# Optimization experiments

Measured on AMD Instinct MI355X. Metric: run time of the kernel, lower is better.

Reference implementation:

```python
import jax, jax.numpy as jnp
import numpy as np

H = 2880      # hidden_size
I = 2880      # intermediate_size
E = 8         # num_experts
K = 4         # experts_per_token
N = 1024      # num tokens
EPS = 1e-5
ALPHA = 1.702
BETA = 1.0


def setup_inputs() -> dict:
    key = jax.random.key(0)
    ks = jax.random.split(key, 8)
    s = 0.02
    return {
        "x": jax.random.normal(ks[0], (N, H), jnp.float32),
        "norm_w": jnp.ones((H,), jnp.float32),
        "gate_w": jax.random.normal(ks[1], (E, H), jnp.float32) * s,
        "gate_b": jax.random.normal(ks[2], (E,), jnp.float32) * s,
        "w_gate_up": jax.random.normal(ks[3], (E, 2 * I, H), jnp.float32) * s,
        "b_gate_up": jax.random.normal(ks[4], (E, 2 * I), jnp.float32) * s,
        "w_down": jax.random.normal(ks[5], (E, H, I), jnp.float32) * s,
        "b_down": jax.random.normal(ks[6], (E, H), jnp.float32) * s,
    }


def reference(x, norm_w, gate_w, gate_b, w_gate_up, b_gate_up, w_down, b_down):
    # RMSNorm
    t = x * jax.lax.rsqrt(jnp.mean(x * x, axis=-1, keepdims=True) + EPS) * norm_w
    # Router gate (Linear with bias)
    logits = t @ gate_w.T + gate_b                      # [N, E]
    # Renormalize routing: top-k of logits, softmax over selected logits
    top_vals, top_idx = jax.lax.top_k(logits, K)        # [N, K]
    route_w = jax.nn.softmax(top_vals, axis=-1)         # [N, K]
    # Dense combine matrix [N, E] (zero for unselected experts)
    n_ar = jnp.arange(N)[:, None]
    R = jnp.zeros((N, E), t.dtype).at[n_ar, top_idx].add(route_w)
    # Fused gate_up projection per expert: [E, N, 2I]
    h = jnp.einsum('nh,eih->eni', t, w_gate_up) + b_gate_up[:, None, :]
    x_glu, x_lin = h[..., :I], h[..., I:]
    # SwiGLU with per-expert alpha/beta (all 1.702 / 1.0)
    act = x_glu * jax.nn.sigmoid(ALPHA * x_glu) * (x_lin + BETA)   # [E, N, I]
    # Down projection per expert: [E, N, H]
    outs = jnp.einsum('eni,ehi->enh', act, w_down) + b_down[:, None, :]
    # Weighted combine over selected experts + residual
    y = jnp.einsum('ne,enh->nh', R, outs)
    return x + y
```

## Files before the change

### kernel.cpp

```cpp
#include <hip/hip_runtime.h>
#include <hip/hip_bf16.h>

#define NTOK 1024
#define HDIM 2880
#define IDIM 2880
#define NEXP 8
#define BK 64
#define NT 45

typedef __attribute__((ext_vector_type(4))) float fx4;
typedef __attribute__((ext_vector_type(8))) short sx8;
typedef __attribute__((ext_vector_type(8))) unsigned short usx8;

typedef const __attribute__((address_space(1))) void* gas_p;
typedef __attribute__((address_space(3))) void* las_p;

__device__ __forceinline__ unsigned short f2bf(float f) {
  __hip_bfloat16 b = __float2bfloat16(f);
  return __builtin_bit_cast(unsigned short, b);
}
__device__ __forceinline__ usx8 cvt8(fx4 a, fx4 b) {
  usx8 u = {f2bf(a.x), f2bf(a.y), f2bf(a.z), f2bf(a.w),
            f2bf(b.x), f2bf(b.y), f2bf(b.z), f2bf(b.w)};
  return u;
}
__device__ __forceinline__ float bf2f(unsigned short u) {
  unsigned v = ((unsigned)u) << 16;
  return __builtin_bit_cast(float, v);
}

#define MFMA16(a, b, c) __builtin_amdgcn_mfma_f32_16x16x32_bf16(a, b, c, 0, 0, 0)

__global__ __launch_bounds__(256) void rms_router_k(
    const float* __restrict__ x, const float* __restrict__ norm_w,
    const float* __restrict__ gate_w, const float* __restrict__ gate_b,
    unsigned short* __restrict__ t_bf, int* __restrict__ cnt,
    int* __restrict__ tok, int* __restrict__ tokE, int* __restrict__ tokS,
    float* __restrict__ tokW) {
  const int n = blockIdx.x;
  const int tid = threadIdx.x;
  const int wid = tid >> 6, lane = tid & 63;
  const float* xr = x + (size_t)n * HDIM;

  float ss = 0.f;
  for (int h = tid; h < HDIM; h += 256) { float v = xr[h]; ss += v * v; }
  #pragma unroll
  for (int o = 32; o > 0; o >>= 1) ss += __shfl_down(ss, o);
  __shared__ float sred[4];
  if (lane == 0) sred[wid] = ss;
  __syncthreads();
  const float rstd =
      rsqrtf((sred[0] + sred[1] + sred[2] + sred[3]) * (1.0f / HDIM) + 1e-5f);

  float p[NEXP];
  #pragma unroll
  for (int e = 0; e < NEXP; e++) p[e] = 0.f;
  for (int h = tid; h < HDIM; h += 256) {
    float xv = xr[h] * norm_w[h];
    t_bf[(size_t)n * HDIM + h] = f2bf(xv * rstd);
    #pragma unroll
    for (int e = 0; e < NEXP; e++) p[e] += xv * gate_w[e * HDIM + h];
  }
  __shared__ float pls[4][NEXP];
  #pragma unroll
  for (int e = 0; e < NEXP; e++) {
    float v = p[e];
    #pragma unroll
    for (int o = 32; o > 0; o >>= 1) v += __shfl_down(v, o);
    if (lane == 0) pls[wid][e] = v;
  }
  __syncthreads();
  if (tid == 0) {
    float lg[NEXP];
    #pragma unroll
    for (int e = 0; e < NEXP; e++)
      lg[e] = (pls[0][e] + pls[1][e] + pls[2][e] + pls[3][e]) * rstd + gate_b[e];
    unsigned used = 0;
    float val[4];
    int idx[4];
    for (int k = 0; k < 4; k++) {
      float best = -1e30f;
      int bi = 0;
      for (int e = 0; e < NEXP; e++)
        if (!((used >> e) & 1u) && lg[e] > best) { best = lg[e]; bi = e; }
      used |= 1u << bi;
      val[k] = best;
      idx[k] = bi;
    }
    float sum = 0.f, w[4];
    for (int k = 0; k < 4; k++) { w[k] = expf(val[k] - val[0]); sum += w[k]; }
    for (int k = 0; k < 4; k++) {
      int e = idx[k];
      int slot = atomicAdd(&cnt[e], 1);
      tok[e * NTOK + slot] = n;
      tokE[n * 4 + k] = e;
      tokS[n * 4 + k] = slot;
      tokW[n * 4 + k] = w[k] / sum;
    }
  }
}

__global__ __launch_bounds__(256) void pack_k(
    const unsigned short* __restrict__ t_bf, const int* __restrict__ cnt,
    const int* __restrict__ tok, unsigned short* __restrict__ a_pack) {
  const int e = blockIdx.x >> 8;
  const int r0 = (blockIdx.x & 255) * 4;
  const int ce = cnt[e];
  const int lim = (ce + 127) & ~127;
  if (r0 >= lim) return;
  const int row = r0 + (threadIdx.x >> 6);
  const int lane = threadIdx.x & 63;
  unsigned short* dst = a_pack + ((size_t)e * NTOK + row) * HDIM;
  if (row < ce) {
    const unsigned short* src = t_bf + (size_t)tok[e * NTOK + row] * HDIM;
    for (int c = lane; c < HDIM / 8; c += 64)
      *(usx8*)(dst + c * 8) = *(const usx8*)(src + c * 8);
  } else {
    const usx8 z = {0, 0, 0, 0, 0, 0, 0, 0};
    for (int c = lane; c < HDIM / 8; c += 64) *(usx8*)(dst + c * 8) = z;
  }
}

__global__ __launch_bounds__(256, 3) void gemm1_k(
    const unsigned short* __restrict__ a_pack,
    const float* __restrict__ w_gate_up, const float* __restrict__ b_gate_up,
    const int* __restrict__ cnt, unsigned short* __restrict__ act_bf) {
  const int h = blockIdx.x;
  const int u = (h >> 6) * 8 + (h & 7);
  const int z = (h >> 3) & 7;
  const int e = u / 45;
  const int c0 = (u % 45) * 64;
  const int m0 = z * 128;
  const int ce = cnt[e];
  if (m0 >= ce) return;

  const int tid = threadIdx.x, lane = tid & 63, wid = tid >> 6;
  const int fr = lane & 15, fq = lane >> 4;
  const int wm = wid >> 1, wn = wid & 1;
  const int sw = ((lane & 7) ^ ((lane >> 3) & 7)) * 8;

  __shared__ __align__(16) unsigned short Ash[128 * 64];
  __shared__ __align__(16) unsigned short Bsh[128 * 64];

  const fx4 FZ = {0.f, 0.f, 0.f, 0.f};
  fx4 accG[4][2], accL[4][2];
  #pragma unroll
  for (int m = 0; m < 4; m++)
    #pragma unroll
    for (int n = 0; n < 2; n++) { accG[m][n] = FZ; accL[m][n] = FZ; }

  const unsigned short* gA[4];
  #pragma unroll
  for (int j = 0; j < 4; ++j) {
    int row = m0 + wid * 32 + j * 8 + (lane >> 3);
    gA[j] = a_pack + ((size_t)e * NTOK + row) * HDIM + sw;
  }
  const float* fB[4];
  int bO[4];
  #pragma unroll
  for (int q = 0; q < 4; ++q) {
    int s = tid + 256 * q;
    int bR = s >> 3, bC = s & 7;
    int wr = bR < 64 ? (c0 + bR) : (IDIM + c0 + (bR - 64));
    fB[q] = w_gate_up + ((size_t)e * (2 * IDIM) + wr) * HDIM + bC * 8;
    bO[q] = bR * 64 + ((bC ^ (bR & 7)) * 8);
  }

  fx4 Ra[8];
  #pragma unroll
  for (int q = 0; q < 4; ++q) {
    Ra[2 * q] = *(const fx4*)(fB[q]);
    Ra[2 * q + 1] = *(const fx4*)(fB[q] + 4);
  }

  for (int t = 0; t < NT; ++t) {
    const int ko = t * BK;
    __syncthreads();
    #pragma unroll
    for (int j = 0; j < 4; ++j)
      __builtin_amdgcn_global_load_lds((gas_p)(gA[j] + ko),
                                       (las_p)&Ash[(wid * 32 + j * 8) * 64], 16,
                                       0, 0);
    #pragma unroll
    for (int q = 0; q < 4; ++q)
      *(usx8*)&Bsh[bO[q]] = cvt8(Ra[2 * q], Ra[2 * q + 1]);
    __syncthreads();
    if (t + 1 < NT) {
      const int kf = (t + 1) * BK;
      #pragma unroll
      for (int q = 0; q < 4; ++q) {
        Ra[2 * q] = *(const fx4*)(fB[q] + kf);
        Ra[2 * q + 1] = *(const fx4*)(fB[q] + kf + 4);
      }
    }
    #pragma unroll
    for (int ks = 0; ks < 2; ++ks) {
      const int off = ((ks * 4 + fq) ^ (fr & 7)) * 8;
      sx8 aF[4], bG[2], bL[2];
      #pragma unroll
      for (int m = 0; m < 4; ++m)
        aF[m] = *(const sx8*)&Ash[(wm * 64 + m * 16 + fr) * 64 + off];
      #pragma unroll
      for (int n = 0; n < 2; ++n) {
        bG[n] = *(const sx8*)&Bsh[(wn * 32 + n * 16 + fr) * 64 + off];
        bL[n] = *(const sx8*)&Bsh[(64 + wn * 32 + n * 16 + fr) * 64 + off];
      }
      __builtin_amdgcn_s_setprio(1);
      #pragma unroll
      for (int n = 0; n < 2; ++n)
        #pragma unroll
        for (int m = 0; m < 4; ++m) {
          accG[m][n] = MFMA16(aF[m], bG[n], accG[m][n]);
          accL[m][n] = MFMA16(aF[m], bL[n], accL[m][n]);
        }
      __builtin_amdgcn_s_setprio(0);
    }
  }

  #pragma unroll
  for (int n = 0; n < 2; ++n) {
    const int col = c0 + wn * 32 + n * 16 + fr;
    const float bg = b_gate_up[e * (2 * IDIM) + col];
    const float bl = b_gate_up[e * (2 * IDIM) + IDIM + col];
    #pragma unroll
    for (int m = 0; m < 4; ++m) {
      #pragma unroll
      for (int r = 0; r < 4; ++r) {
        int slot = m0 + wm * 64 + m * 16 + fq * 4 + r;
        if (slot < ce) {
          float gv = accG[m][n][r] + bg;
          float lv = accL[m][n][r] + bl;
          float a = gv * (1.0f / (1.0f + __expf(-1.702f * gv))) * (lv + 1.0f);
          act_bf[((size_t)e * NTOK + slot) * IDIM + col] = f2bf(a);
        }
      }
    }
  }
}

__global__ __launch_bounds__(256, 3) void gemm2_k(
    const unsigned short* __restrict__ act_bf, const float* __restrict__ w_down,
    const float* __restrict__ b_down, const int* __restrict__ cnt,
    unsigned short* __restrict__ outs_bf) {
  const int h = blockIdx.x;
  const int u = (h >> 6) * 8 + (h & 7);
  const int z = (h >> 3) & 7;
  const int e = u / 30;
  const int c0 = (u % 30) * 96;
  const int m0 = z * 128;
  const int ce = cnt[e];
  if (m0 >= ce) return;

  const int tid = threadIdx.x, lane = tid & 63, wid = tid >> 6;
  const int fr = lane & 15, fq = lane >> 4;
  const int wm = wid >> 1, wn = wid & 1;
  const int sw = ((lane & 7) ^ ((lane >> 3) & 7)) * 8;

  __shared__ __align__(16) unsigned short Ash[128 * 64];
  __shared__ __align__(16) unsigned short Bsh[96 * 64];

  const fx4 FZ = {0.f, 0.f, 0.f, 0.f};
  fx4 acc[4][3];
  #pragma unroll
  for (int m = 0; m < 4; m++)
    #pragma unroll
    for (int n = 0; n < 3; n++) acc[m][n] = FZ;

  const unsigned short* gA[4];
  #pragma unroll
  for (int j = 0; j < 4; ++j) {
    int row = m0 + wid * 32 + j * 8 + (lane >> 3);
    gA[j] = act_bf + ((size_t)e * NTOK + row) * IDIM + sw;
  }
  const float* fB[3];
  int bO[3];
  #pragma unroll
  for (int q = 0; q < 3; ++q) {
    int s = tid + 256 * q;
    int bR = s >> 3, bC = s & 7;
    fB[q] = w_down + ((size_t)e * HDIM + c0 + bR) * IDIM + bC * 8;
    bO[q] = bR * 64 + ((bC ^ (bR & 7)) * 8);
  }

  fx4 Ra[6];
  #pragma unroll
  for (int q = 0; q < 3; ++q) {
    Ra[2 * q] = *(const fx4*)(fB[q]);
    Ra[2 * q + 1] = *(const fx4*)(fB[q] + 4);
  }

  for (int t = 0; t < NT; ++t) {
    const int ko = t * BK;
    __syncthreads();
    #pragma unroll
    for (int j = 0; j < 4; ++j)
      __builtin_amdgcn_global_load_lds((gas_p)(gA[j] + ko),
                                       (las_p)&Ash[(wid * 32 + j * 8) * 64], 16,
                                       0, 0);
    #pragma unroll
    for (int q = 0; q < 3; ++q)
      *(usx8*)&Bsh[bO[q]] = cvt8(Ra[2 * q], Ra[2 * q + 1]);
    __syncthreads();
    if (t + 1 < NT) {
      const int kf = (t + 1) * BK;
      #pragma unroll
      for (int q = 0; q < 3; ++q) {
        Ra[2 * q] = *(const fx4*)(fB[q] + kf);
        Ra[2 * q + 1] = *(const fx4*)(fB[q] + kf + 4);
      }
    }
    #pragma unroll
    for (int ks = 0; ks < 2; ++ks) {
      const int off = ((ks * 4 + fq) ^ (fr & 7)) * 8;
      sx8 aF[4], bB[3];
      #pragma unroll
      for (int m = 0; m < 4; ++m)
        aF[m] = *(const sx8*)&Ash[(wm * 64 + m * 16 + fr) * 64 + off];
      #pragma unroll
      for (int n = 0; n < 3; ++n)
        bB[n] = *(const sx8*)&Bsh[(wn * 48 + n * 16 + fr) * 64 + off];
      __builtin_amdgcn_s_setprio(1);
      #pragma unroll
      for (int n = 0; n < 3; ++n)
        #pragma unroll
        for (int m = 0; m < 4; ++m)
          acc[m][n] = MFMA16(aF[m], bB[n], acc[m][n]);
      __builtin_amdgcn_s_setprio(0);
    }
  }

  #pragma unroll
  for (int n = 0; n < 3; ++n) {
    const int col = c0 + wn * 48 + n * 16 + fr;
    const float bias = b_down[e * HDIM + col];
    #pragma unroll
    for (int m = 0; m < 4; ++m) {
      #pragma unroll
      for (int r = 0; r < 4; ++r) {
        int slot = m0 + wm * 64 + m * 16 + fq * 4 + r;
        if (slot < ce)
          outs_bf[((size_t)e * NTOK + slot) * HDIM + col] =
              f2bf(acc[m][n][r] + bias);
      }
    }
  }
}

__global__ __launch_bounds__(256) void combine_k(
    const float* __restrict__ x, const unsigned short* __restrict__ outs_bf,
    const int* __restrict__ tokE, const int* __restrict__ tokS,
    const float* __restrict__ tokW, float* __restrict__ out) {
  const int n = blockIdx.x;
  const unsigned short* src[4];
  float w[4];
  #pragma unroll
  for (int k = 0; k < 4; ++k) {
    int e = tokE[n * 4 + k], s = tokS[n * 4 + k];
    w[k] = tokW[n * 4 + k];
    src[k] = outs_bf + ((size_t)e * NTOK + s) * HDIM;
  }
  const float* xr = x + (size_t)n * HDIM;
  float* orow = out + (size_t)n * HDIM;
  for (int c = threadIdx.x; c < HDIM / 8; c += 256) {
    fx4 lo = *(const fx4*)(xr + c * 8);
    fx4 hi = *(const fx4*)(xr + c * 8 + 4);
    #pragma unroll
    for (int k = 0; k < 4; ++k) {
      usx8 v = *(const usx8*)(src[k] + c * 8);
      lo.x += w[k] * bf2f(v[0]);
      lo.y += w[k] * bf2f(v[1]);
      lo.z += w[k] * bf2f(v[2]);
      lo.w += w[k] * bf2f(v[3]);
      hi.x += w[k] * bf2f(v[4]);
      hi.y += w[k] * bf2f(v[5]);
      hi.z += w[k] * bf2f(v[6]);
      hi.w += w[k] * bf2f(v[7]);
    }
    *(fx4*)(orow + c * 8) = lo;
    *(fx4*)(orow + c * 8 + 4) = hi;
  }
}

extern "C" void kernel_launch(void* const* d_in, const int* in_sizes, int n_in,
                              void* d_out, int out_size, void* d_ws,
                              size_t ws_size, hipStream_t stream) {
  const float* x = (const float*)d_in[0];
  const float* norm_w = (const float*)d_in[1];
  const float* gate_w = (const float*)d_in[2];
  const float* gate_b = (const float*)d_in[3];
  const float* w_gate_up = (const float*)d_in[4];
  const float* b_gate_up = (const float*)d_in[5];
  const float* w_down = (const float*)d_in[6];
  const float* b_down = (const float*)d_in[7];
  float* out = (float*)d_out;

  char* ws = (char*)d_ws;
  size_t off = 0;
  unsigned short* t_bf = (unsigned short*)(ws + off);
  off += (size_t)NTOK * HDIM * 2;
  unsigned short* a_pack = (unsigned short*)(ws + off);
  off += (size_t)NEXP * NTOK * HDIM * 2;
  unsigned short* act_bf = (unsigned short*)(ws + off);
  off += (size_t)NEXP * NTOK * IDIM * 2;
  unsigned short* outs_bf = (unsigned short*)(ws + off);
  off += (size_t)NEXP * NTOK * HDIM * 2;
  int* cnt = (int*)(ws + off);
  off += 256;
  int* tok = (int*)(ws + off);
  off += (size_t)NEXP * NTOK * 4;
  int* tokE = (int*)(ws + off);
  off += (size_t)NTOK * 4 * 4;
  int* tokS = (int*)(ws + off);
  off += (size_t)NTOK * 4 * 4;
  float* tokW = (float*)(ws + off);
  off += (size_t)NTOK * 4 * 4;

  hipMemsetAsync(cnt, 0, NEXP * sizeof(int), stream);
  rms_router_k<<<NTOK, 256, 0, stream>>>(x, norm_w, gate_w, gate_b, t_bf, cnt,
                                         tok, tokE, tokS, tokW);
  pack_k<<<NEXP * 256, 256, 0, stream>>>(t_bf, cnt, tok, a_pack);
  gemm1_k<<<2880, 256, 0, stream>>>(a_pack, w_gate_up, b_gate_up, cnt, act_bf);
  gemm2_k<<<1920, 256, 0, stream>>>(act_bf, w_down, b_down, cnt, outs_bf);
  combine_k<<<NTOK, 256, 0, stream>>>(x, outs_bf, tokE, tokS, tokW, out);
}
```

Baseline: 561.8 us.

## Double-buffer LDS and enlarge MoE GEMM tiles to 256 rows with 512 threads

```diff
diff --git a/kernel.cpp b/kernel.cpp
--- a/kernel.cpp
+++ b/kernel.cpp
@@ -121,16 +121,15 @@
   }
 }
 
-__global__ __launch_bounds__(256, 3) void gemm1_k(
+__global__ __launch_bounds__(512, 1) void gemm1_k(
     const unsigned short* __restrict__ a_pack,
     const float* __restrict__ w_gate_up, const float* __restrict__ b_gate_up,
     const int* __restrict__ cnt, unsigned short* __restrict__ act_bf) {
   const int h = blockIdx.x;
-  const int u = (h >> 6) * 8 + (h & 7);
-  const int z = (h >> 3) & 7;
-  const int e = u / 45;
-  const int c0 = (u % 45) * 64;
-  const int m0 = z * 128;
+  const int s = h / 3, z = h - s * 3;
+  const int e = s / 45;
+  const int c0 = (s % 45) * 64;
+  const int m0 = z * 256;
   const int ce = cnt[e];
   if (m0 >= ce) return;
 
@@ -139,8 +138,8 @@
   const int wm = wid >> 1, wn = wid & 1;
   const int sw = ((lane & 7) ^ ((lane >> 3) & 7)) * 8;
 
-  __shared__ __align__(16) unsigned short Ash[128 * 64];
-  __shared__ __align__(16) unsigned short Bsh[128 * 64];
+  __shared__ __align__(16) unsigned short Ash[2][256 * 64];
+  __shared__ __align__(16) unsigned short Bsh[2][128 * 64];
 
   const fx4 FZ = {0.f, 0.f, 0.f, 0.f};
   fx4 accG[4][2], accL[4][2];
@@ -155,66 +154,76 @@
     int row = m0 + wid * 32 + j * 8 + (lane >> 3);
     gA[j] = a_pack + ((size_t)e * NTOK + row) * HDIM + sw;
   }
-  const float* fB[4];
-  int bO[4];
-  #pragma unroll
-  for (int q = 0; q < 4; ++q) {
-    int s = tid + 256 * q;
-    int bR = s >> 3, bC = s & 7;
+  const float* fB[2];
+  int bO[2];
+  #pragma unroll
+  for (int q = 0; q < 2; ++q) {
+    int sl = tid + 512 * q;
+    int bR = sl >> 3, bC = sl & 7;
     int wr = bR < 64 ? (c0 + bR) : (IDIM + c0 + (bR - 64));
     fB[q] = w_gate_up + ((size_t)e * (2 * IDIM) + wr) * HDIM + bC * 8;
     bO[q] = bR * 64 + ((bC ^ (bR & 7)) * 8);
   }
 
-  fx4 Ra[8];
-  #pragma unroll
-  for (int q = 0; q < 4; ++q) {
-    Ra[2 * q] = *(const fx4*)(fB[q]);
-    Ra[2 * q + 1] = *(const fx4*)(fB[q] + 4);
-  }
-
+  fx4 Ra[4];
+  #define G1_DMA_A(kt, bb)                                                     \
+    {                                                                          \
+      _Pragma("unroll") for (int j = 0; j < 4; ++j)                            \
+          __builtin_amdgcn_global_load_lds(                                    \
+              (gas_p)(gA[j] + (size_t)(kt)*BK),                                \
+              (las_p)&Ash[bb][(wid * 32 + j * 8) * 64], 16, 0, 0);             \
+    }
+  #define G1_LOADB(kt)                                                         \
+    {                                                                          \
+      _Pragma("unroll") for (int q = 0; q < 2; ++q) {                          \
+        Ra[2 * q] = *(const fx4*)(fB[q] + (size_t)(kt)*BK);                    \
+        Ra[2 * q + 1] = *(const fx4*)(fB[q] + (size_t)(kt)*BK + 4);            \
+      }                                                                        \
+    }
+  #define G1_WRITEB(bb)                                                        \
+    {                                                                          \
+      _Pragma("unroll") for (int q = 0; q < 2; ++q)                            \
+          *(usx8*)&Bsh[bb][bO[q]] = cvt8(Ra[2 * q], Ra[2 * q + 1]);            \
+    }
+  #define G1_COMPUTE(bb)                                                       \
+    {                                                                          \
+      _Pragma("unroll") for (int ks = 0; ks < 2; ++ks) {                       \
+        const int off = ((ks * 4 + fq) ^ (fr & 7)) * 8;                        \
+        sx8 aF[4], bG[2], bL[2];                                               \
+        _Pragma("unroll") for (int m = 0; m < 4; ++m) aF[m] =                  \
+            *(const sx8*)&Ash[bb][(wm * 64 + m * 16 + fr) * 64 + off];         \
+        _Pragma("unroll") for (int n = 0; n < 2; ++n) {                        \
+          bG[n] = *(const sx8*)&Bsh[bb][(wn * 32 + n * 16 + fr) * 64 + off];   \
+          bL[n] =                                                              \
+              *(const sx8*)&Bsh[bb][(64 + wn * 32 + n * 16 + fr) * 64 + off];  \
+        }                                                                      \
+        __builtin_amdgcn_s_setprio(1);                                         \
+        _Pragma("unroll") for (int n = 0; n < 2; ++n)                          \
+            _Pragma("unroll") for (int m = 0; m < 4; ++m) {                    \
+          accG[m][n] = MFMA16(aF[m], bG[n], accG[m][n]);                       \
+          accL[m][n] = MFMA16(aF[m], bL[n], accL[m][n]);                       \
+        }                                                                      \
+        __builtin_amdgcn_s_setprio(0);                                         \
+      }                                                                        \
+    }
+
+  G1_DMA_A(0, 0);
+  G1_LOADB(0);
+  G1_WRITEB(0);
+  G1_DMA_A(1, 1);
+  G1_LOADB(1);
+  __syncthreads();
+
+  int cur = 0;
   for (int t = 0; t < NT; ++t) {
-    const int ko = t * BK;
+    G1_COMPUTE(cur);
+    if (t + 1 < NT) G1_WRITEB(cur ^ 1);
     __syncthreads();
-    #pragma unroll
-    for (int j = 0; j < 4; ++j)
-      __builtin_amdgcn_global_load_lds((gas_p)(gA[j] + ko),
-                                       (las_p)&Ash[(wid * 32 + j * 8) * 64], 16,
-                                       0, 0);
-    #pragma unroll
-    for (int q = 0; q < 4; ++q)
-      *(usx8*)&Bsh[bO[q]] = cvt8(Ra[2 * q], Ra[2 * q + 1]);
-    __syncthreads();
-    if (t + 1 < NT) {
-      const int kf = (t + 1) * BK;
-      #pragma unroll
-      for (int q = 0; q < 4; ++q) {
-        Ra[2 * q] = *(const fx4*)(fB[q] + kf);
-        Ra[2 * q + 1] = *(const fx4*)(fB[q] + kf + 4);
-      }
-    }
-    #pragma unroll
-    for (int ks = 0; ks < 2; ++ks) {
-      const int off = ((ks * 4 + fq) ^ (fr & 7)) * 8;
-      sx8 aF[4], bG[2], bL[2];
-      #pragma unroll
-      for (int m = 0; m < 4; ++m)
-        aF[m] = *(const sx8*)&Ash[(wm * 64 + m * 16 + fr) * 64 + off];
-      #pragma unroll
-      for (int n = 0; n < 2; ++n) {
-        bG[n] = *(const sx8*)&Bsh[(wn * 32 + n * 16 + fr) * 64 + off];
-        bL[n] = *(const sx8*)&Bsh[(64 + wn * 32 + n * 16 + fr) * 64 + off];
-      }
-      __builtin_amdgcn_s_setprio(1);
-      #pragma unroll
-      for (int n = 0; n < 2; ++n)
-        #pragma unroll
-        for (int m = 0; m < 4; ++m) {
-          accG[m][n] = MFMA16(aF[m], bG[n], accG[m][n]);
-          accL[m][n] = MFMA16(aF[m], bL[n], accL[m][n]);
-        }
-      __builtin_amdgcn_s_setprio(0);
-    }
+    if (t + 2 < NT) {
+      G1_DMA_A(t + 2, cur);
+      G1_LOADB(t + 2);
+    }
+    cur ^= 1;
   }
 
   #pragma unroll
@@ -238,16 +247,15 @@
   }
 }
 
-__global__ __launch_bounds__(256, 3) void gemm2_k(
+__global__ __launch_bounds__(512, 1) void gemm2_k(
     const unsigned short* __restrict__ act_bf, const float* __restrict__ w_down,
     const float* __restrict__ b_down, const int* __restrict__ cnt,
     unsigned short* __restrict__ outs_bf) {
   const int h = blockIdx.x;
-  const int u = (h >> 6) * 8 + (h & 7);
-  const int z = (h >> 3) & 7;
-  const int e = u / 30;
-  const int c0 = (u % 30) * 96;
-  const int m0 = z * 128;
+  const int s = h / 3, z = h - s * 3;
+  const int e = s / 30;
+  const int c0 = (s % 30) * 96;
+  const int m0 = z * 256;
   const int ce = cnt[e];
   if (m0 >= ce) return;
 
@@ -256,8 +264,8 @@
   const int wm = wid >> 1, wn = wid & 1;
   const int sw = ((lane & 7) ^ ((lane >> 3) & 7)) * 8;
 
-  __shared__ __align__(16) unsigned short Ash[128 * 64];
-  __shared__ __align__(16) unsigned short Bsh[96 * 64];
+  __shared__ __align__(16) unsigned short Ash[2][256 * 64];
+  __shared__ __align__(16) unsigned short Bsh[2][96 * 64];
 
   const fx4 FZ = {0.f, 0.f, 0.f, 0.f};
   fx4 acc[4][3];
@@ -272,61 +280,71 @@
     int row = m0 + wid * 32 + j * 8 + (lane >> 3);
     gA[j] = act_bf + ((size_t)e * NTOK + row) * IDIM + sw;
   }
-  const float* fB[3];
-  int bO[3];
-  #pragma unroll
-  for (int q = 0; q < 3; ++q) {
-    int s = tid + 256 * q;
-    int bR = s >> 3, bC = s & 7;
-    fB[q] = w_down + ((size_t)e * HDIM + c0 + bR) * IDIM + bC * 8;
-    bO[q] = bR * 64 + ((bC ^ (bR & 7)) * 8);
-  }
-
-  fx4 Ra[6];
-  #pragma unroll
-  for (int q = 0; q < 3; ++q) {
-    Ra[2 * q] = *(const fx4*)(fB[q]);
-    Ra[2 * q + 1] = *(const fx4*)(fB[q] + 4);
-  }
-
+  const int bR0 = tid >> 3, bC0 = tid & 7;
+  const int s1 = tid + 512;
+  const int bR1 = s1 >> 3, bC1 = s1 & 7;
+  const float* wb = w_down + (size_t)e * HDIM * IDIM;
+  const float* fB0 = wb + (size_t)(c0 + bR0) * IDIM + bC0 * 8;
+  const float* fB1 = wb + (size_t)(c0 + bR1) * IDIM + bC1 * 8;
+  const int bO0 = bR0 * 64 + ((bC0 ^ (bR0 & 7)) * 8);
+  const int bO1 = bR1 * 64 + ((bC1 ^ (bR1 & 7)) * 8);
+
+  fx4 Ra[4];
+  #define G2_DMA_A(kt, bb)                                                     \
+    {                                                                          \
+      _Pragma("unroll") for (int j = 0; j < 4; ++j)                            \
+          __builtin_amdgcn_global_load_lds(                                    \
+              (gas_p)(gA[j] + (size_t)(kt)*BK),                                \
+              (las_p)&Ash[bb][(wid * 32 + j * 8) * 64], 16, 0, 0);             \
+    }
+  #define G2_LOADB(kt)                                                         \
+    {                                                                          \
+      Ra[0] = *(const fx4*)(fB0 + (size_t)(kt)*BK);                            \
+      Ra[1] = *(const fx4*)(fB0 + (size_t)(kt)*BK + 4);                        \
+      if (tid < 256) {                                                         \
+        Ra[2] = *(const fx4*)(fB1 + (size_t)(kt)*BK);                          \
+        Ra[3] = *(const fx4*)(fB1 + (size_t)(kt)*BK + 4);                      \
+      }                                                                        \
+    }
+  #define G2_WRITEB(bb)                                                        \
+    {                                                                          \
+      *(usx8*)&Bsh[bb][bO0] = cvt8(Ra[0], Ra[1]);                              \
+      if (tid < 256) *(usx8*)&Bsh[bb][bO1] = cvt8(Ra[2], Ra[3]);               \
+    }
+  #define G2_COMPUTE(bb)                                                       \
+    {                                                                          \
+      _Pragma("unroll") for (int ks = 0; ks < 2; ++ks) {                       \
+        const int off = ((ks * 4 + fq) ^ (fr & 7)) * 8;                        \
+        sx8 aF[4], bB[3];                                                      \
+        _Pragma("unroll") for (int m = 0; m < 4; ++m) aF[m] =                  \
+            *(const sx8*)&Ash[bb][(wm * 64 + m * 16 + fr) * 64 + off];         \
+        _Pragma("unroll") for (int n = 0; n < 3; ++n) bB[n] =                  \
+            *(const sx8*)&Bsh[bb][(wn * 48 + n * 16 + fr) * 64 + off];         \
+        __builtin_amdgcn_s_setprio(1);                                         \
+        _Pragma("unroll") for (int n = 0; n < 3; ++n)                          \
+            _Pragma("unroll") for (int m = 0; m < 4; ++m)                      \
+                acc[m][n] = MFMA16(aF[m], bB[n], acc[m][n]);                   \
+        __builtin_amdgcn_s_setprio(0);                                         \
+      }                                                                        \
+    }
+
+  G2_DMA_A(0, 0);
+  G2_LOADB(0);
+  G2_WRITEB(0);
+  G2_DMA_A(1, 1);
+  G2_LOADB(1);
+  __syncthreads();
+
+  int cur = 0;
   for (int t = 0; t < NT; ++t) {
-    const int ko = t * BK;
+    G2_COMPUTE(cur);
+    if (t + 1 < NT) G2_WRITEB(cur ^ 1);
     __syncthreads();
-    #pragma unroll
-    for (int j = 0; j < 4; ++j)
-      __builtin_amdgcn_global_load_lds((gas_p)(gA[j] + ko),
-                                       (las_p)&Ash[(wid * 32 + j * 8) * 64], 16,
-                                       0, 0);
-    #pragma unroll
-    for (int q = 0; q < 3; ++q)
-      *(usx8*)&Bsh[bO[q]] = cvt8(Ra[2 * q], Ra[2 * q + 1]);
-    __syncthreads();
-    if (t + 1 < NT) {
-      const int kf = (t + 1) * BK;
-      #pragma unroll
-      for (int q = 0; q < 3; ++q) {
-        Ra[2 * q] = *(const fx4*)(fB[q] + kf);
-        Ra[2 * q + 1] = *(const fx4*)(fB[q] + kf + 4);
-      }
-    }
-    #pragma unroll
-    for (int ks = 0; ks < 2; ++ks) {
-      const int off = ((ks * 4 + fq) ^ (fr & 7)) * 8;
-      sx8 aF[4], bB[3];
-      #pragma unroll
-      for (int m = 0; m < 4; ++m)
-        aF[m] = *(const sx8*)&Ash[(wm * 64 + m * 16 + fr) * 64 + off];
-      #pragma unroll
-      for (int n = 0; n < 3; ++n)
-        bB[n] = *(const sx8*)&Bsh[(wn * 48 + n * 16 + fr) * 64 + off];
-      __builtin_amdgcn_s_setprio(1);
-      #pragma unroll
-      for (int n = 0; n < 3; ++n)
-        #pragma unroll
-        for (int m = 0; m < 4; ++m)
-          acc[m][n] = MFMA16(aF[m], bB[n], acc[m][n]);
-      __builtin_amdgcn_s_setprio(0);
-    }
+    if (t + 2 < NT) {
+      G2_DMA_A(t + 2, cur);
+      G2_LOADB(t + 2);
+    }
+    cur ^= 1;
   }
 
   #pragma unroll
@@ -419,7 +437,8 @@
   rms_router_k<<<NTOK, 256, 0, stream>>>(x, norm_w, gate_w, gate_b, t_bf, cnt,
                                          tok, tokE, tokS, tokW);
   pack_k<<<NEXP * 256, 256, 0, stream>>>(t_bf, cnt, tok, a_pack);
-  gemm1_k<<<2880, 256, 0, stream>>>(a_pack, w_gate_up, b_gate_up, cnt, act_bf);
-  gemm2_k<<<1920, 256, 0, stream>>>(act_bf, w_down, b_down, cnt, outs_bf);
+  gemm1_k<<<360 * 3, 512, 0, stream>>>(a_pack, w_gate_up, b_gate_up, cnt,
+                                       act_bf);
+  gemm2_k<<<240 * 3, 512, 0, stream>>>(act_bf, w_down, b_down, cnt, outs_bf);
   combine_k<<<NTOK, 256, 0, stream>>>(x, outs_bf, tokE, tokS, tokW, out);
 }
```

Result: slower. 704.0 us (+25.3%).

## Switch expert GEMMs to 32x32x16 MFMA and shrink gemm2 N-tile

Applied to the files above, without the earlier changes.

```diff
diff --git a/kernel.cpp b/kernel.cpp
--- a/kernel.cpp
+++ b/kernel.cpp
@@ -9,6 +9,7 @@
 #define NT 45
 
 typedef __attribute__((ext_vector_type(4))) float fx4;
+typedef __attribute__((ext_vector_type(16))) float fx16;
 typedef __attribute__((ext_vector_type(8))) short sx8;
 typedef __attribute__((ext_vector_type(8))) unsigned short usx8;
 
@@ -29,7 +30,7 @@
   return __builtin_bit_cast(float, v);
 }
 
-#define MFMA16(a, b, c) __builtin_amdgcn_mfma_f32_16x16x32_bf16(a, b, c, 0, 0, 0)
+#define MFMA32(a, b, c) __builtin_amdgcn_mfma_f32_32x32x16_bf16(a, b, c, 0, 0, 0)
 
 __global__ __launch_bounds__(256) void rms_router_k(
     const float* __restrict__ x, const float* __restrict__ norm_w,
@@ -134,25 +135,23 @@
   const int ce = cnt[e];
   if (m0 >= ce) return;
 
-  const int tid = threadIdx.x, lane = tid & 63, wid = tid >> 6;
-  const int fr = lane & 15, fq = lane >> 4;
+  const int tid = threadIdx.x, l = tid & 63, wid = tid >> 6;
   const int wm = wid >> 1, wn = wid & 1;
-  const int sw = ((lane & 7) ^ ((lane >> 3) & 7)) * 8;
+  const int l7 = l & 7, koct = l >> 5, l31 = l & 31;
+  const int sw = (l7 ^ ((l >> 3) & 7)) * 8;
 
   __shared__ __align__(16) unsigned short Ash[128 * 64];
   __shared__ __align__(16) unsigned short Bsh[128 * 64];
 
-  const fx4 FZ = {0.f, 0.f, 0.f, 0.f};
-  fx4 accG[4][2], accL[4][2];
-  #pragma unroll
-  for (int m = 0; m < 4; m++)
-    #pragma unroll
-    for (int n = 0; n < 2; n++) { accG[m][n] = FZ; accL[m][n] = FZ; }
+  const fx16 FZ16 = {0.f, 0.f, 0.f, 0.f, 0.f, 0.f, 0.f, 0.f,
+                     0.f, 0.f, 0.f, 0.f, 0.f, 0.f, 0.f, 0.f};
+  fx16 accG[2], accL[2];
+  accG[0] = FZ16; accG[1] = FZ16; accL[0] = FZ16; accL[1] = FZ16;
 
   const unsigned short* gA[4];
   #pragma unroll
   for (int j = 0; j < 4; ++j) {
-    int row = m0 + wid * 32 + j * 8 + (lane >> 3);
+    int row = m0 + wid * 32 + j * 8 + (l >> 3);
     gA[j] = a_pack + ((size_t)e * NTOK + row) * HDIM + sw;
   }
   const float* fB[4];
@@ -194,45 +193,38 @@
       }
     }
     #pragma unroll
-    for (int ks = 0; ks < 2; ++ks) {
-      const int off = ((ks * 4 + fq) ^ (fr & 7)) * 8;
-      sx8 aF[4], bG[2], bL[2];
-      #pragma unroll
-      for (int m = 0; m < 4; ++m)
-        aF[m] = *(const sx8*)&Ash[(wm * 64 + m * 16 + fr) * 64 + off];
-      #pragma unroll
-      for (int n = 0; n < 2; ++n) {
-        bG[n] = *(const sx8*)&Bsh[(wn * 32 + n * 16 + fr) * 64 + off];
-        bL[n] = *(const sx8*)&Bsh[(64 + wn * 32 + n * 16 + fr) * 64 + off];
+    for (int ks = 0; ks < 4; ++ks) {
+      const int c = ks * 2 + koct;
+      const int off = (c ^ l7) * 8;
+      sx8 aF[2], bG, bL;
+      #pragma unroll
+      for (int mb = 0; mb < 2; ++mb)
+        aF[mb] = *(const sx8*)&Ash[(wm * 64 + mb * 32 + l31) * 64 + off];
+      bG = *(const sx8*)&Bsh[(wn * 32 + l31) * 64 + off];
+      bL = *(const sx8*)&Bsh[(64 + wn * 32 + l31) * 64 + off];
+      __builtin_amdgcn_s_setprio(1);
+      #pragma unroll
+      for (int mb = 0; mb < 2; ++mb) {
+        accG[mb] = MFMA32(aF[mb], bG, accG[mb]);
+        accL[mb] = MFMA32(aF[mb], bL, accL[mb]);
       }
-      __builtin_amdgcn_s_setprio(1);
-      #pragma unroll
-      for (int n = 0; n < 2; ++n)
-        #pragma unroll
-        for (int m = 0; m < 4; ++m) {
-          accG[m][n] = MFMA16(aF[m], bG[n], accG[m][n]);
-          accL[m][n] = MFMA16(aF[m], bL[n], accL[m][n]);
-        }
       __builtin_amdgcn_s_setprio(0);
     }
   }
 
-  #pragma unroll
-  for (int n = 0; n < 2; ++n) {
-    const int col = c0 + wn * 32 + n * 16 + fr;
-    const float bg = b_gate_up[e * (2 * IDIM) + col];
-    const float bl = b_gate_up[e * (2 * IDIM) + IDIM + col];
-    #pragma unroll
-    for (int m = 0; m < 4; ++m) {
-      #pragma unroll
-      for (int r = 0; r < 4; ++r) {
-        int slot = m0 + wm * 64 + m * 16 + fq * 4 + r;
-        if (slot < ce) {
-          float gv = accG[m][n][r] + bg;
-          float lv = accL[m][n][r] + bl;
-          float a = gv * (1.0f / (1.0f + __expf(-1.702f * gv))) * (lv + 1.0f);
-          act_bf[((size_t)e * NTOK + slot) * IDIM + col] = f2bf(a);
-        }
+  const int col = c0 + wn * 32 + l31;
+  const float bg = b_gate_up[e * (2 * IDIM) + col];
+  const float bl = b_gate_up[e * (2 * IDIM) + IDIM + col];
+  #pragma unroll
+  for (int mb = 0; mb < 2; ++mb) {
+    #pragma unroll
+    for (int r = 0; r < 16; ++r) {
+      int slot = m0 + wm * 64 + mb * 32 + (r & 3) + 8 * (r >> 2) + 4 * koct;
+      if (slot < ce) {
+        float gv = accG[mb][r] + bg;
+        float lv = accL[mb][r] + bl;
+        float a = gv * (1.0f / (1.0f + __expf(-1.702f * gv))) * (lv + 1.0f);
+        act_bf[((size_t)e * NTOK + slot) * IDIM + col] = f2bf(a);
       }
     }
   }
@@ -245,46 +237,44 @@
   const int h = blockIdx.x;
   const int u = (h >> 6) * 8 + (h & 7);
   const int z = (h >> 3) & 7;
-  const int e = u / 30;
-  const int c0 = (u % 30) * 96;
+  const int e = u / 45;
+  const int c0 = (u % 45) * 64;
   const int m0 = z * 128;
   const int ce = cnt[e];
   if (m0 >= ce) return;
 
-  const int tid = threadIdx.x, lane = tid & 63, wid = tid >> 6;
-  const int fr = lane & 15, fq = lane >> 4;
+  const int tid = threadIdx.x, l = tid & 63, wid = tid >> 6;
   const int wm = wid >> 1, wn = wid & 1;
-  const int sw = ((lane & 7) ^ ((lane >> 3) & 7)) * 8;
+  const int l7 = l & 7, koct = l >> 5, l31 = l & 31;
+  const int sw = (l7 ^ ((l >> 3) & 7)) * 8;
 
   __shared__ __align__(16) unsigned short Ash[128 * 64];
-  __shared__ __align__(16) unsigned short Bsh[96 * 64];
-
-  const fx4 FZ = {0.f, 0.f, 0.f, 0.f};
-  fx4 acc[4][3];
-  #pragma unroll
-  for (int m = 0; m < 4; m++)
-    #pragma unroll
-    for (int n = 0; n < 3; n++) acc[m][n] = FZ;
+  __shared__ __align__(16) unsigned short Bsh[64 * 64];
+
+  const fx16 FZ16 = {0.f, 0.f, 0.f, 0.f, 0.f, 0.f, 0.f, 0.f,
+                     0.f, 0.f, 0.f, 0.f, 0.f, 0.f, 0.f, 0.f};
+  fx16 acc[2];
+  acc[0] = FZ16; acc[1] = FZ16;
 
   const unsigned short* gA[4];
   #pragma unroll
   for (int j = 0; j < 4; ++j) {
-    int row = m0 + wid * 32 + j * 8 + (lane >> 3);
+    int row = m0 + wid * 32 + j * 8 + (l >> 3);
     gA[j] = act_bf + ((size_t)e * NTOK + row) * IDIM + sw;
   }
-  const float* fB[3];
-  int bO[3];
-  #pragma unroll
-  for (int q = 0; q < 3; ++q) {
+  const float* fB[2];
+  int bO[2];
+  #pragma unroll
+  for (int q = 0; q < 2; ++q) {
     int s = tid + 256 * q;
     int bR = s >> 3, bC = s & 7;
     fB[q] = w_down + ((size_t)e * HDIM + c0 + bR) * IDIM + bC * 8;
     bO[q] = bR * 64 + ((bC ^ (bR & 7)) * 8);
   }
 
-  fx4 Ra[6];
-  #pragma unroll
-  for (int q = 0; q < 3; ++q) {
+  fx4 Ra[4];
+  #pragma unroll
+  for (int q = 0; q < 2; ++q) {
     Ra[2 * q] = *(const fx4*)(fB[q]);
     Ra[2 * q + 1] = *(const fx4*)(fB[q] + 4);
   }
@@ -298,50 +288,43 @@
                                        (las_p)&Ash[(wid * 32 + j * 8) * 64], 16,
                                        0, 0);
     #pragma unroll
-    for (int q = 0; q < 3; ++q)
+    for (int q = 0; q < 2; ++q)
       *(usx8*)&Bsh[bO[q]] = cvt8(Ra[2 * q], Ra[2 * q + 1]);
     __syncthreads();
     if (t + 1 < NT) {
       const int kf = (t + 1) * BK;
       #pragma unroll
-      for (int q = 0; q < 3; ++q) {
+      for (int q = 0; q < 2; ++q) {
         Ra[2 * q] = *(const fx4*)(fB[q] + kf);
         Ra[2 * q + 1] = *(const fx4*)(fB[q] + kf + 4);
       }
     }
     #pragma unroll
-    for (int ks = 0; ks < 2; ++ks) {
-      const int off = ((ks * 4 + fq) ^ (fr & 7)) * 8;
-      sx8 aF[4], bB[3];
-      #pragma unroll
-      for (int m = 0; m < 4; ++m)
-        aF[m] = *(const sx8*)&Ash[(wm * 64 + m * 16 + fr) * 64 + off];
-      #pragma unroll
-      for (int n = 0; n < 3; ++n)
-        bB[n] = *(const sx8*)&Bsh[(wn * 48 + n * 16 + fr) * 64 + off];
+    for (int ks = 0; ks < 4; ++ks) {
+      const int c = ks * 2 + koct;
+      const int off = (c ^ l7) * 8;
+      sx8 aF[2], bB;
+      #pragma unroll
+      for (int mb = 0; mb < 2; ++mb)
+        aF[mb] = *(const sx8*)&Ash[(wm * 64 + mb * 32 + l31) * 64 + off];
+      bB = *(const sx8*)&Bsh[(wn * 32 + l31) * 64 + off];
       __builtin_amdgcn_s_setprio(1);
       #pragma unroll
-      for (int n = 0; n < 3; ++n)
-        #pragma unroll
-        for (int m = 0; m < 4; ++m)
-          acc[m][n] = MFMA16(aF[m], bB[n], acc[m][n]);
+      for (int mb = 0; mb < 2; ++mb) acc[mb] = MFMA32(aF[mb], bB, acc[mb]);
       __builtin_amdgcn_s_setprio(0);
     }
   }
 
-  #pragma unroll
-  for (int n = 0; n < 3; ++n) {
-    const int col = c0 + wn * 48 + n * 16 + fr;
-    const float bias = b_down[e * HDIM + col];
-    #pragma unroll
-    for (int m = 0; m < 4; ++m) {
-      #pragma unroll
-      for (int r = 0; r < 4; ++r) {
-        int slot = m0 + wm * 64 + m * 16 + fq * 4 + r;
-        if (slot < ce)
-          outs_bf[((size_t)e * NTOK + slot) * HDIM + col] =
-              f2bf(acc[m][n][r] + bias);
-      }
+  const int col = c0 + wn * 32 + l31;
+  const float bias = b_down[e * HDIM + col];
+  #pragma unroll
+  for (int mb = 0; mb < 2; ++mb) {
+    #pragma unroll
+    for (int r = 0; r < 16; ++r) {
+      int slot = m0 + wm * 64 + mb * 32 + (r & 3) + 8 * (r >> 2) + 4 * koct;
+      if (slot < ce)
+        outs_bf[((size_t)e * NTOK + slot) * HDIM + col] =
+            f2bf(acc[mb][r] + bias);
     }
   }
 }
@@ -420,6 +403,6 @@
                                          tok, tokE, tokS, tokW);
   pack_k<<<NEXP * 256, 256, 0, stream>>>(t_bf, cnt, tok, a_pack);
   gemm1_k<<<2880, 256, 0, stream>>>(a_pack, w_gate_up, b_gate_up, cnt, act_bf);
-  gemm2_k<<<1920, 256, 0, stream>>>(act_bf, w_down, b_down, cnt, outs_bf);
+  gemm2_k<<<2880, 256, 0, stream>>>(act_bf, w_down, b_down, cnt, outs_bf);
   combine_k<<<NTOK, 256, 0, stream>>>(x, outs_bf, tokE, tokS, tokW, out);
 }
```

Measured after the change: 589.9 us. 1.05x slower.
